# Kernel optimization log

Hardware: AMD Instinct MI355X
Metric: run time of the kernel (lower is better)

The kernel has to match this reference:

```python
import jax, jax.numpy as jnp
import numpy as np
import math

B, S = 2, 2048
IN_FEATURES = 4096
OUT_FEATURES = 4096
BLOCK_SIZE = 64
NUM_FFT_MATRICES = 4
IN_BLOCKS = IN_FEATURES // BLOCK_SIZE
OUT_BLOCKS = OUT_FEATURES // BLOCK_SIZE  # 64


def setup_inputs() -> dict:
    key = jax.random.key(0)
    k1, k2 = jax.random.split(key)
    scale = 1.0 / math.sqrt(BLOCK_SIZE * IN_BLOCKS)
    x = jax.random.normal(k1, (B, S, IN_FEATURES), dtype=jnp.float32)
    circulant_params = jax.random.normal(
        k2, (NUM_FFT_MATRICES, OUT_BLOCKS, IN_BLOCKS, BLOCK_SIZE), dtype=jnp.float32) * scale
    channel_weights = jnp.ones((NUM_FFT_MATRICES,), dtype=jnp.float32) / NUM_FFT_MATRICES
    return {"x": x, "circulant_params": circulant_params, "channel_weights": channel_weights}


def reference(x, circulant_params, channel_weights):
    b, s, in_feat = x.shape
    # split channels into circulant blocks: (b, s, in_blocks, block)
    x_blocks = x.reshape(b, s, IN_BLOCKS, BLOCK_SIZE)
    x_fft = jnp.fft.rfft(x_blocks, axis=-1)                    # (b, s, i, F) complex
    circ_fft = jnp.fft.rfft(circulant_params, axis=-1)         # (m, o, i, F) complex
    # channel-weighted combine over the m fft matrices (linear, so fold into weights)
    circ_w = jnp.einsum('m,moif->oif', channel_weights.astype(circ_fft.dtype), circ_fft)
    # per-frequency complex contraction over in_blocks (the block-circulant matmul)
    y_fft = jnp.einsum('bsif,oif->bsof', x_fft, circ_w)        # (b, s, o, F)
    y = jnp.fft.irfft(y_fft, n=BLOCK_SIZE, axis=-1)            # (b, s, o, block)
    return y.reshape(b, s, OUT_FEATURES).astype(x.dtype)
```

## Files before the change

kernel.cpp:

```cpp
#include <hip/hip_runtime.h>
#include <math.h>


typedef unsigned short u16;
typedef unsigned int   u32;
typedef __attribute__((ext_vector_type(8))) short bf16x8;
typedef __attribute__((ext_vector_type(4))) float f32x4;

#define TWO_PI 6.2831853071795864769f

#define SF 2056
#define BF_ELEMS (33u*128u*128u)
#define DT_OFF   BF_ELEMS
#define DT_ELEMS (2u*4u*80u*8u)
#define E_OFF    (DT_OFF + DT_ELEMS)
#define E_ELEMS  (3u*4u*64u*8u)

__device__ __forceinline__ u16 f2bf(float f) {
    union { float f; unsigned u; } v; v.f = f;
    unsigned r = v.u + 0x7FFFu + ((v.u >> 16) & 1u);
    return (u16)(r >> 16);
}

__global__ void prep(const float* __restrict__ p, const float* __restrict__ cw,
                     u16* __restrict__ Bf, u16* __restrict__ Dt, u16* __restrict__ E) {
    const int tid = threadIdx.x;
    if (blockIdx.x == 0) {
        for (int e = tid; e < (int)DT_ELEMS; e += 256) {
            int j = e & 7, rowid = e >> 3;
            int n = rowid % 80, grp = rowid / 80;
            int k = (grp >> 2) * 32 + (grp & 3) * 8 + j;
            float v = 0.f;
            if (n < 66) {
                int f = n >> 1;
                float ang = TWO_PI * (float)((f * k) & 63) * (1.f / 64.f);
                v = (n & 1) ? -sinf(ang) : cosf(ang);
            }
            Dt[e] = f2bf(v);
        }
        for (int e = tid; e < (int)E_ELEMS; e += 256) {
            int j = e & 7, rowid = e >> 3;
            int t = rowid % 64, grp = rowid / 64;
            int k = (grp >> 2) * 32 + (grp & 3) * 8 + j;
            float v = 0.f;
            if (k < 66) {
                int f = k >> 1;
                float wf = (f == 0 || f == 32) ? 1.f : 2.f;
                float ang = TWO_PI * (float)((f * t) & 63) * (1.f / 64.f);
                v = (wf * (1.f / 64.f)) * ((k & 1) ? -sinf(ang) : cosf(ang));
            }
            E[e] = f2bf(v);
        }
        return;
    }
    __shared__ float  ct[4][64];
    __shared__ float2 trig[64];
    const int pr = tid >> 6, ln = tid & 63;
    if (tid < 64) {
        float s, c;
        sincosf(TWO_PI * (float)tid * (1.f / 64.f), &s, &c);
        trig[tid] = make_float2(s, c);
    }
    const int pg = (blockIdx.x - 1) * 4 + pr;
    const int o = pg >> 6, i = pg & 63;
    {
        const float* base = p + (size_t)o * 4096 + i * 64 + ln;
        ct[pr][ln] = cw[0] * base[0]      + cw[1] * base[262144]
                   + cw[2] * base[524288] + cw[3] * base[786432];
    }
    __syncthreads();
    if (ln < 33) {
        float cr = 0.f, ci = 0.f;
        for (int u = 0; u < 64; ++u) {
            float2 sc = trig[(ln * u) & 63];
            cr += ct[pr][u] * sc.y; ci -= ct[pr][u] * sc.x;
        }
        u16* b = Bf + (size_t)ln * 16384 + (2 * o) * 128 + 2 * i;
        b[0]   = f2bf(cr);  b[1]   = f2bf(-ci);
        b[128] = f2bf(ci);  b[129] = f2bf(cr);
    }
}

__global__ __launch_bounds__(1024) void fused(const float* __restrict__ x,
                                              const u16* __restrict__ Dt,
                                              const u16* __restrict__ Bf,
                                              const u16* __restrict__ E2,
                                              float* __restrict__ y) {
    __shared__ u16 sm[33 * SF];
    const int tid = threadIdx.x, lane = tid & 63, wave = tid >> 6;
    const int lm = lane & 15, q = lane >> 4, kq8 = q * 8, r0 = q * 4;
    const float* xb = x + (size_t)blockIdx.x * (16u * 4096u);

    {
        f32x4 acc[4][5];
#pragma unroll
        for (int mi = 0; mi < 4; ++mi)
#pragma unroll
            for (int ni = 0; ni < 5; ++ni) acc[mi][ni] = (f32x4){0.f,0.f,0.f,0.f};
#pragma unroll
        for (int kt = 0; kt < 2; ++kt) {
            bf16x8 bfr[5];
#pragma unroll
            for (int ni = 0; ni < 5; ++ni)
                bfr[ni] = *(const bf16x8*)&Dt[((kt*4 + q)*80 + ni*16 + lm)*8];
#pragma unroll
            for (int mi = 0; mi < 4; ++mi) {
                const int row = wave*64 + mi*16 + lm;
                const float* rp = xb + row*64 + kt*32 + kq8;
                float4 p0 = *(const float4*)rp;
                float4 p1 = *(const float4*)(rp + 4);
                union { u16 u[8]; bf16x8 v; } pk;
                pk.u[0]=f2bf(p0.x); pk.u[1]=f2bf(p0.y);
                pk.u[2]=f2bf(p0.z); pk.u[3]=f2bf(p0.w);
                pk.u[4]=f2bf(p1.x); pk.u[5]=f2bf(p1.y);
                pk.u[6]=f2bf(p1.z); pk.u[7]=f2bf(p1.w);
#pragma unroll
                for (int ni = 0; ni < 5; ++ni)
                    acc[mi][ni] = __builtin_amdgcn_mfma_f32_16x16x32_bf16(
                        pk.v, bfr[ni], acc[mi][ni], 0, 0, 0);
            }
        }
        const int sw = (wave & 7) << 3;
#pragma unroll
        for (int mi = 0; mi < 4; ++mi)
#pragma unroll
            for (int ni = 0; ni < 5; ++ni) {
                const int col = ni*16 + lm;
                if (col < 66) {
                    const int f = col >> 1, par = col & 1;
                    f32x4 v = acc[mi][ni];
#pragma unroll
                    for (int r = 0; r < 4; ++r) {
                        int ii = mi*16 + r0 + r;
                        sm[f*SF + wave*128 + (((ii<<1)|par) ^ sw)] = f2bf(v[r]);
                    }
                }
            }
    }
    __syncthreads();

    for (int f = wave; f < 33; f += 16) {
        u16* sl = &sm[f * SF];
        const u16* Bff = Bf + (size_t)f * 16384;
        bf16x8 af[4];
#pragma unroll
        for (int ks = 0; ks < 4; ++ks)
            af[ks] = *(const bf16x8*)&sl[lm*128 + ((ks*32 + kq8) ^ ((lm&7)<<3))];
#pragma unroll
        for (int nt = 0; nt < 8; ++nt) {
            f32x4 c = (f32x4){0.f,0.f,0.f,0.f};
#pragma unroll
            for (int ks = 0; ks < 4; ++ks) {
                bf16x8 bq = *(const bf16x8*)&Bff[(nt*16 + lm)*128 + ks*32 + kq8];
                c = __builtin_amdgcn_mfma_f32_16x16x32_bf16(af[ks], bq, c, 0, 0, 0);
            }
#pragma unroll
            for (int r = 0; r < 4; ++r) {
                int tok = r0 + r;
                sl[tok*128 + ((nt*16 + lm) ^ ((tok&7)<<3))] = f2bf(c[r]);
            }
        }
    }
    __syncthreads();

    bf16x8 ef[3][4];
#pragma unroll
    for (int kt = 0; kt < 3; ++kt)
#pragma unroll
        for (int mt = 0; mt < 4; ++mt)
            ef[kt][mt] = *(const bf16x8*)&E2[((kt*4 + q)*64 + mt*16 + lm)*8];
    const int tokL = wave;
    const int swc = (tokL & 7) << 3;
#pragma unroll
    for (int nt = 0; nt < 4; ++nt) {
        const int o = nt*16 + lm;
        const int cb = tokL*128 + ((2*o) ^ swc);
        f32x4 acc[4];
#pragma unroll
        for (int mt = 0; mt < 4; ++mt) acc[mt] = (f32x4){0.f,0.f,0.f,0.f};
#pragma unroll
        for (int kt = 0; kt < 3; ++kt) {
            union { u32 w[4]; bf16x8 v; } bq;
#pragma unroll
            for (int j = 0; j < 4; ++j) {
                int f = kt*16 + q*4 + j;
                u32 vv = 0u;
                if (f < 33) vv = *(const u32*)&sm[f*SF + cb];
                bq.w[j] = vv;
            }
#pragma unroll
            for (int mt = 0; mt < 4; ++mt)
                acc[mt] = __builtin_amdgcn_mfma_f32_16x16x32_bf16(
                    ef[kt][mt], bq.v, acc[mt], 0, 0, 0);
        }
        float* yb = y + ((size_t)(blockIdx.x*16 + tokL))*4096 + o*64;
#pragma unroll
        for (int mt = 0; mt < 4; ++mt) {
            float4 st = { acc[mt][0], acc[mt][1], acc[mt][2], acc[mt][3] };
            *(float4*)&yb[mt*16 + r0] = st;
        }
    }
}

extern "C" void kernel_launch(void* const* d_in, const int* in_sizes, int n_in,
                              void* d_out, int out_size, void* d_ws, size_t ws_size,
                              hipStream_t stream) {
    const float* x      = (const float*)d_in[0];
    const float* params = (const float*)d_in[1];
    const float* cw     = (const float*)d_in[2];
    float* out = (float*)d_out;

    u16* Bf = (u16*)d_ws;
    u16* Dt = Bf + DT_OFF;
    u16* Eg = Bf + E_OFF;

    prep<<<1025, 256, 0, stream>>>(params, cw, Bf, Dt, Eg);
    fused<<<256, 1024, 0, stream>>>(x, Dt, Bf, Eg, out);
}
```

Before: 161.5 us.

## Halve tokens per block and rebalance frequency work across eight waves

The fused kernel now handles 8 tokens per block with 512 threads instead of 16 tokens with 1024 threads. It launches 512 blocks and uses half the shared memory per block. The per-frequency GEMM stage is rescheduled so each wave does four frequencies, and the leftover frequency 32 is split across waves by output tile. Only the valid half of the 16-row MFMA tile (8 tokens) is written back. The aim is better occupancy and load balance across CUs, at the cost of wasting half of each MFMA's rows and reloading B fragments from global twice as often.

```diff
diff --git a/kernel.cpp b/kernel.cpp
--- a/kernel.cpp
+++ b/kernel.cpp
@@ -9,7 +9,7 @@
 
 #define TWO_PI 6.2831853071795864769f
 
-#define SF 2056
+#define SF 1032
 #define BF_ELEMS (33u*128u*128u)
 #define DT_OFF   BF_ELEMS
 #define DT_ELEMS (2u*4u*80u*8u)
@@ -81,15 +81,15 @@
     }
 }
 
-__global__ __launch_bounds__(1024) void fused(const float* __restrict__ x,
-                                              const u16* __restrict__ Dt,
-                                              const u16* __restrict__ Bf,
-                                              const u16* __restrict__ E2,
-                                              float* __restrict__ y) {
+__global__ __launch_bounds__(512, 4) void fused(const float* __restrict__ x,
+                                                const u16* __restrict__ Dt,
+                                                const u16* __restrict__ Bf,
+                                                const u16* __restrict__ E2,
+                                                float* __restrict__ y) {
     __shared__ u16 sm[33 * SF];
     const int tid = threadIdx.x, lane = tid & 63, wave = tid >> 6;
     const int lm = lane & 15, q = lane >> 4, kq8 = q * 8, r0 = q * 4;
-    const float* xb = x + (size_t)blockIdx.x * (16u * 4096u);
+    const float* xb = x + (size_t)blockIdx.x * (8u * 4096u);
 
     {
         f32x4 acc[4][5];
@@ -120,7 +120,7 @@
                         pk.v, bfr[ni], acc[mi][ni], 0, 0, 0);
             }
         }
-        const int sw = (wave & 7) << 3;
+        const int sw = wave << 3;
 #pragma unroll
         for (int mi = 0; mi < 4; ++mi)
 #pragma unroll
@@ -139,13 +139,37 @@
     }
     __syncthreads();
 
-    for (int f = wave; f < 33; f += 16) {
+    {
+        u16* sl = &sm[32 * SF];
+        const u16* Bff = Bf + (size_t)32 * 16384;
+        bf16x8 af[4];
+#pragma unroll
+        for (int ks = 0; ks < 4; ++ks)
+            af[ks] = *(const bf16x8*)&sl[(lm&7)*128 + ((ks*32 + kq8) ^ ((lm&7)<<3))];
+        __syncthreads();
+        const int nt = wave;
+        f32x4 c = (f32x4){0.f,0.f,0.f,0.f};
+#pragma unroll
+        for (int ks = 0; ks < 4; ++ks) {
+            bf16x8 bq = *(const bf16x8*)&Bff[(nt*16 + lm)*128 + ks*32 + kq8];
+            c = __builtin_amdgcn_mfma_f32_16x16x32_bf16(af[ks], bq, c, 0, 0, 0);
+        }
+        if (q < 2)
+#pragma unroll
+            for (int r = 0; r < 4; ++r) {
+                int tok = r0 + r;
+                sl[tok*128 + ((nt*16 + lm) ^ (tok<<3))] = f2bf(c[r]);
+            }
+    }
+#pragma unroll
+    for (int t = 0; t < 4; ++t) {
+        const int f = wave + t*8;
         u16* sl = &sm[f * SF];
         const u16* Bff = Bf + (size_t)f * 16384;
         bf16x8 af[4];
 #pragma unroll
         for (int ks = 0; ks < 4; ++ks)
-            af[ks] = *(const bf16x8*)&sl[lm*128 + ((ks*32 + kq8) ^ ((lm&7)<<3))];
+            af[ks] = *(const bf16x8*)&sl[(lm&7)*128 + ((ks*32 + kq8) ^ ((lm&7)<<3))];
 #pragma unroll
         for (int nt = 0; nt < 8; ++nt) {
             f32x4 c = (f32x4){0.f,0.f,0.f,0.f};
@@ -154,11 +178,12 @@
                 bf16x8 bq = *(const bf16x8*)&Bff[(nt*16 + lm)*128 + ks*32 + kq8];
                 c = __builtin_amdgcn_mfma_f32_16x16x32_bf16(af[ks], bq, c, 0, 0, 0);
             }
-#pragma unroll
-            for (int r = 0; r < 4; ++r) {
-                int tok = r0 + r;
-                sl[tok*128 + ((nt*16 + lm) ^ ((tok&7)<<3))] = f2bf(c[r]);
-            }
+            if (q < 2)
+#pragma unroll
+                for (int r = 0; r < 4; ++r) {
+                    int tok = r0 + r;
+                    sl[tok*128 + ((nt*16 + lm) ^ (tok<<3))] = f2bf(c[r]);
+                }
         }
     }
     __syncthreads();
@@ -170,7 +195,7 @@
         for (int mt = 0; mt < 4; ++mt)
             ef[kt][mt] = *(const bf16x8*)&E2[((kt*4 + q)*64 + mt*16 + lm)*8];
     const int tokL = wave;
-    const int swc = (tokL & 7) << 3;
+    const int swc = tokL << 3;
 #pragma unroll
     for (int nt = 0; nt < 4; ++nt) {
         const int o = nt*16 + lm;
@@ -193,7 +218,7 @@
                 acc[mt] = __builtin_amdgcn_mfma_f32_16x16x32_bf16(
                     ef[kt][mt], bq.v, acc[mt], 0, 0, 0);
         }
-        float* yb = y + ((size_t)(blockIdx.x*16 + tokL))*4096 + o*64;
+        float* yb = y + ((size_t)(blockIdx.x*8 + tokL))*4096 + o*64;
 #pragma unroll
         for (int mt = 0; mt < 4; ++mt) {
             float4 st = { acc[mt][0], acc[mt][1], acc[mt][2], acc[mt][3] };
@@ -215,5 +240,5 @@
     u16* Eg = Bf + E_OFF;
 
     prep<<<1025, 256, 0, stream>>>(params, cw, Bf, Dt, Eg);
-    fused<<<256, 1024, 0, stream>>>(x, Dt, Bf, Eg, out);
-}
+    fused<<<512, 512, 0, stream>>>(x, Dt, Bf, Eg, out);
+}
```

Measured after the change: 186.7 us. +15.6%, slower.
